# Performance work log

Measured on AMD Instinct MI355X. Metric: run time of the kernel, lower is better.

Reference implementation:

```python
import jax, jax.numpy as jnp
import numpy as np


def setup_inputs() -> dict:
    key = jax.random.key(0)
    ks = jax.random.split(key, 9)
    B, C, H, W = 8, 512, 56, 56
    E = 256  # embed_dim = in_channels / r
    s = 0.02
    return {
        "x": jax.random.normal(ks[0], (B, C, H, W), dtype=jnp.float32),
        "wq": jax.random.normal(ks[1], (E, C), dtype=jnp.float32) * s,
        "bq": jax.random.normal(ks[2], (E,), dtype=jnp.float32) * s,
        "wk": jax.random.normal(ks[3], (E, C), dtype=jnp.float32) * s,
        "bk": jax.random.normal(ks[4], (E,), dtype=jnp.float32) * s,
        "wv": jax.random.normal(ks[5], (E, C), dtype=jnp.float32) * s,
        "bv": jax.random.normal(ks[6], (E,), dtype=jnp.float32) * s,
        "wo": jax.random.normal(ks[7], (C, E), dtype=jnp.float32) * s,
        "bo": jax.random.normal(ks[8], (C,), dtype=jnp.float32) * s,
    }


def reference(x, wq, bq, wk, bk, wv, bv, wo, bo):
    B, C, H, W = x.shape
    N = H * W
    # 1x1 convs == per-pixel linear projections; flatten spatial dims
    xf = x.reshape(B, C, N)                                   # b c n
    q = jnp.einsum("ec,bcn->bne", wq, xf) + bq                # b n e
    k = jnp.einsum("ec,bcn->ben", wk, xf) + bk[None, :, None] # b e n
    v = jnp.einsum("ec,bcn->bne", wv, xf) + bv                # b n e
    attn = jnp.einsum("bne,bem->bnm", q, k) / N               # b n n (unnormalized, /N scale)
    embed = jnp.einsum("bnm,bme->bne", attn, v)               # b n e
    out = jnp.einsum("ce,bne->bcn", wo, embed) + bo[None, :, None]
    return out.reshape(B, C, H, W) + x
```

## Files before the change

kernel.cpp:

```cpp
#include <hip/hip_runtime.h>
#include <hip/hip_bf16.h>


typedef __attribute__((ext_vector_type(8))) __bf16 bf16x8;
typedef __attribute__((ext_vector_type(4))) float floatx4;

struct __align__(8) bh4 { __hip_bfloat16 x, y, z, w; };
struct __align__(16) bh8 { __hip_bfloat16 h[8]; };

__device__ __forceinline__ void load_lds16(const void* g, void* l) {
    __builtin_amdgcn_global_load_lds((const __attribute__((address_space(1))) void*)g,
                                     (__attribute__((address_space(3))) void*)l, 16, 0, 0);
}

__global__ __launch_bounds__(256)
void prep_all(const float* __restrict__ wo, const float* __restrict__ wv,
              const float* __restrict__ wq, const float* __restrict__ wk,
              const float* __restrict__ bq, const float* __restrict__ bk,
              const float* __restrict__ bv,
              __hip_bfloat16* __restrict__ Pdb, __hip_bfloat16* __restrict__ Qtb,
              float* __restrict__ u, float* __restrict__ r, float* __restrict__ w,
              float* __restrict__ kap, float* __restrict__ sv)
{
    const int tid = threadIdx.x;
    if (blockIdx.z == 2) {
        int blk = blockIdx.y * 8 + blockIdx.x;
        if (blk < 2) {
            int c = blk * 256 + tid;
            float su = 0.f, sr = 0.f, sw = 0.f;
            for (int e = 0; e < 256; ++e) {
                su = fmaf(wo[(long long)c * 256 + e], bv[e], su);
                sr = fmaf(bk[e], wq[(long long)e * 512 + c], sr);
                sw = fmaf(wk[(long long)e * 512 + c], bq[e], sw);
            }
            u[c] = su; r[c] = sr; w[c] = sw;
            if (c == 0) {
                float k2 = 0.f;
                for (int e = 0; e < 256; ++e) k2 = fmaf(bk[e], bq[e], k2);
                *kap = k2;
            }
        } else if (blk == 2) {
            float4* p = (float4*)sv;
            for (int i = tid; i < 1024; i += 256) p[i] = make_float4(0.f, 0.f, 0.f, 0.f);
        }
        return;
    }
    __shared__ __align__(16) float As[16][68];
    __shared__ __align__(16) float Bs[16][68];
    const int tx = tid & 15, ty = tid >> 4;
    const int m0 = blockIdx.y * 64, n0 = blockIdx.x * 64;
    const bool doQ = (blockIdx.z == 1);
    const int lk = tid >> 4, lc = (tid & 15) * 4;
    const int lr = tid >> 2, lk4 = (tid & 3) * 4;
    float acc[4][4] = {};
    for (int k0 = 0; k0 < 256; k0 += 16) {
        float4 av, bv4;
        if (doQ) {
            av = *(const float4*)&wq[(long long)(k0 + lk) * 512 + m0 + lc];
            bv4 = *(const float4*)&wk[(long long)(k0 + lk) * 512 + n0 + lc];
        } else {
            av = *(const float4*)&wo[(long long)(m0 + lr) * 256 + k0 + lk4];
            bv4 = *(const float4*)&wv[(long long)(k0 + lk) * 512 + n0 + lc];
        }
        __syncthreads();
        if (doQ) {
            *(float4*)&As[lk][lc] = av;
        } else {
            As[lk4 + 0][lr] = av.x; As[lk4 + 1][lr] = av.y;
            As[lk4 + 2][lr] = av.z; As[lk4 + 3][lr] = av.w;
        }
        *(float4*)&Bs[lk][lc] = bv4;
        __syncthreads();
#pragma unroll
        for (int kk = 0; kk < 16; ++kk) {
            float a[4], b[4];
#pragma unroll
            for (int i = 0; i < 4; ++i) { a[i] = As[kk][ty * 4 + i]; b[i] = Bs[kk][tx * 4 + i]; }
#pragma unroll
            for (int i = 0; i < 4; ++i)
#pragma unroll
                for (int j = 0; j < 4; ++j) acc[i][j] = fmaf(a[i], b[j], acc[i][j]);
        }
    }
    const int mo = m0 + ty * 4, no = n0 + tx * 4;
    if (doQ) {
#pragma unroll
        for (int i = 0; i < 4; ++i)
#pragma unroll
            for (int j = 0; j < 4; ++j)
                Qtb[(long long)(mo + i) * 512 + no + j] = __float2bfloat16(acc[i][j]);
    } else {
#pragma unroll
        for (int i = 0; i < 4; ++i)
#pragma unroll
            for (int j = 0; j < 4; ++j) {
                __hip_bfloat16 v = __float2bfloat16(acc[i][j]);
                Pdb[(long long)(mo + i) * 1024 + no + j] = v;
                Pdb[(long long)(mo + i) * 1024 + no + j + 512] = v;
            }
    }
}

__global__ __launch_bounds__(256)
void transpose_conv(const float* __restrict__ x, __hip_bfloat16* __restrict__ xT,
                    __hip_bfloat16* __restrict__ xnp, float* __restrict__ s)
{
    __shared__ float t[64][65];
    const int b = blockIdx.z;
    const int n0 = blockIdx.x * 64, c0 = blockIdx.y * 64;
    const int tid = threadIdx.x;
    const int nch = tid & 7;
    const int cr  = tid >> 3;
    __hip_bfloat16* xTo = xT + (long long)b * 3200 * 512;
    __hip_bfloat16* xno = xnp + (long long)b * 512 * 3200;

    if (n0 >= 3136) {
        bh8 z8;
#pragma unroll
        for (int k = 0; k < 8; ++k) z8.h[k] = __float2bfloat16(0.f);
#pragma unroll
        for (int pass = 0; pass < 2; ++pass) {
            int rr = cr + 32 * pass;
            *(bh8*)&xno[(long long)(c0 + rr) * 3200 + n0 + nch * 8] = z8;
            *(bh8*)&xTo[(long long)(n0 + rr) * 512 + c0 + nch * 8] = z8;
        }
        return;
    }
    const float* xb = x + (long long)b * 512 * 3136;
#pragma unroll
    for (int pass = 0; pass < 2; ++pass) {
        const int cl = cr + 32 * pass;
        const int c = c0 + cl;
        const float* xr = xb + (long long)c * 3136 + n0 + nch * 8;
        float4 v0 = *(const float4*)xr;
        float4 v1 = *(const float4*)(xr + 4);
        bh8 o;
        o.h[0] = __float2bfloat16(v0.x); o.h[1] = __float2bfloat16(v0.y);
        o.h[2] = __float2bfloat16(v0.z); o.h[3] = __float2bfloat16(v0.w);
        o.h[4] = __float2bfloat16(v1.x); o.h[5] = __float2bfloat16(v1.y);
        o.h[6] = __float2bfloat16(v1.z); o.h[7] = __float2bfloat16(v1.w);
        *(bh8*)&xno[(long long)c * 3200 + n0 + nch * 8] = o;
        const int nl = nch * 8;
        t[nl + 0][cl] = v0.x; t[nl + 1][cl] = v0.y;
        t[nl + 2][cl] = v0.z; t[nl + 3][cl] = v0.w;
        t[nl + 4][cl] = v1.x; t[nl + 5][cl] = v1.y;
        t[nl + 6][cl] = v1.z; t[nl + 7][cl] = v1.w;
        float rs = v0.x + v0.y + v0.z + v0.w + v1.x + v1.y + v1.z + v1.w;
        rs += __shfl_xor(rs, 1, 8);
        rs += __shfl_xor(rs, 2, 8);
        rs += __shfl_xor(rs, 4, 8);
        if (nch == 0) atomicAdd(&s[b * 512 + c], rs);
    }
    __syncthreads();
#pragma unroll
    for (int pass = 0; pass < 2; ++pass) {
        const int nl = cr + 32 * pass;
        const int cc = nch * 8;
        bh8 o;
#pragma unroll
        for (int k = 0; k < 8; ++k) o.h[k] = __float2bfloat16(t[nl][cc + k]);
        *(bh8*)&xTo[(long long)(n0 + nl) * 512 + c0 + cc] = o;
    }
}

__global__ __launch_bounds__(256)
void vec2_kernel(const __hip_bfloat16* __restrict__ T, const __hip_bfloat16* __restrict__ Pdb,
                 const __hip_bfloat16* __restrict__ Qtb, const float* __restrict__ s,
                 const float* __restrict__ u, const float* __restrict__ w,
                 const float* __restrict__ kap, const float* __restrict__ bo,
                 float* __restrict__ ps, float* __restrict__ sq, float* __restrict__ a2)
{
    const int idx = blockIdx.x * 4 + (threadIdx.x >> 6);
    const int lane = threadIdx.x & 63;
    const int b = idx >> 9, c = idx & 511;
    const int j0 = lane * 8;
    const float* sb = s + b * 512;
    float4 s0 = *(const float4*)&sb[j0], s1 = *(const float4*)&sb[j0 + 4];
    float4 w0 = *(const float4*)&w[j0],  w1 = *(const float4*)&w[j0 + 4];
    bf16x8 pv = *(const bf16x8*)&Pdb[(long long)c * 1024 + j0];
    bf16x8 qv = *(const bf16x8*)&Qtb[(long long)c * 512 + j0];
    bf16x8 tv = *(const bf16x8*)&T[(long long)b * 262144 + (long long)c * 512 + j0];
    float sj[8] = {s0.x, s0.y, s0.z, s0.w, s1.x, s1.y, s1.z, s1.w};
    float wj[8] = {w0.x, w0.y, w0.z, w0.w, w1.x, w1.y, w1.z, w1.w};
    float aps = 0.f, asq = 0.f, atw = 0.f, asw = 0.f;
#pragma unroll
    for (int t = 0; t < 8; ++t) {
        aps = fmaf((float)pv[t], sj[t], aps);
        asq = fmaf((float)qv[t], sj[t], asq);
        atw = fmaf((float)tv[t], wj[t], atw);
        asw = fmaf(sj[t], wj[t], asw);
    }
#pragma unroll
    for (int m = 1; m < 64; m <<= 1) {
        aps += __shfl_xor(aps, m);
        asq += __shfl_xor(asq, m);
        atw += __shfl_xor(atw, m);
        asw += __shfl_xor(asw, m);
    }
    if (lane == 0) {
        ps[idx] = aps; sq[idx] = asq;
        float kp = *kap;
        a2[idx] = (atw + u[c] * asw + aps * kp) * (1.f / 3136.f) + u[c] * kp + bo[c];
    }
}

#define SWZ64(row) ((row) & 7)

__global__ __launch_bounds__(256)
void mfma_g(const __hip_bfloat16* __restrict__ A, long long sA, int lda,
            __hip_bfloat16* __restrict__ C, long long sC, int ldc,
            int kLen)
{
    constexpr int BKT = 64;
    constexpr int CPR = BKT / 8;
    constexpr int NC = 64 * CPR / 256;
    __shared__ __hip_bfloat16 As[64 * BKT];
    __shared__ __hip_bfloat16 Bs[64 * BKT];
    const int tid = threadIdx.x;
    const int lane = tid & 63;
    const int w = tid >> 6;
    const int wm = (w >> 1) << 5;
    const int wn = (w & 1) << 5;
    const int ln = lane & 15;
    const int hi = lane >> 4;
    const int bx = blockIdx.x;
    const int batch = bx & 7, ks = bx >> 3;
    int p = blockIdx.y, mt = 0;
    while (p >= 8 - mt) { p -= 8 - mt; ++mt; }
    const int nt = mt + p;
    const int m0 = mt << 6, n0 = nt << 6;
    const long long k0 = (long long)ks * kLen;

    const __hip_bfloat16* gA[NC];
    const __hip_bfloat16* gB[NC];
#pragma unroll
    for (int q0 = 0; q0 < NC; ++q0) {
        int q = tid + 256 * q0;
        int row = q / CPR;
        int c = (q % CPR) ^ SWZ64(row);
        gA[q0] = A + batch * sA + (long long)(m0 + row) * lda + k0 + c * 8;
        gB[q0] = A + batch * sA + (long long)(n0 + row) * lda + k0 + c * 8;
    }
    floatx4 acc[2][2] = {};
    const int nK = kLen / BKT;
    for (int kt = 0; kt < nK; ++kt) {
#pragma unroll
        for (int q0 = 0; q0 < NC; ++q0) {
            load_lds16(gA[q0], As + (tid + 256 * q0) * 8);
            load_lds16(gB[q0], Bs + (tid + 256 * q0) * 8);
            gA[q0] += BKT; gB[q0] += BKT;
        }
        __syncthreads();
#pragma unroll
        for (int kk = 0; kk < BKT / 32; ++kk) {
            const int cidx = kk * 4 + hi;
            bf16x8 af[2], bfr[2];
#pragma unroll
            for (int i = 0; i < 2; ++i) {
                int row = wm + i * 16 + ln;
                af[i] = *(const bf16x8*)(As + row * BKT + ((cidx ^ SWZ64(row)) << 3));
            }
#pragma unroll
            for (int j = 0; j < 2; ++j) {
                int row = wn + j * 16 + ln;
                bfr[j] = *(const bf16x8*)(Bs + row * BKT + ((cidx ^ SWZ64(row)) << 3));
            }
#pragma unroll
            for (int i = 0; i < 2; ++i)
#pragma unroll
                for (int j = 0; j < 2; ++j)
                    acc[i][j] = __builtin_amdgcn_mfma_f32_16x16x32_bf16(af[i], bfr[j], acc[i][j], 0, 0, 0);
        }
        __syncthreads();
    }

    __hip_bfloat16* Cb = C + batch * sC + ks * 512;
#pragma unroll
    for (int i = 0; i < 2; ++i) {
        int mb = m0 + wm + i * 16 + hi * 4;
#pragma unroll
        for (int j = 0; j < 2; ++j) {
            int nl = n0 + wn + j * 16 + ln;
            bh4 mv;
            mv.x = __float2bfloat16(acc[i][j][0]);
            mv.y = __float2bfloat16(acc[i][j][1]);
            mv.z = __float2bfloat16(acc[i][j][2]);
            mv.w = __float2bfloat16(acc[i][j][3]);
            Cb[(long long)(mb + 0) * ldc + nl] = mv.x;
            Cb[(long long)(mb + 1) * ldc + nl] = mv.y;
            Cb[(long long)(mb + 2) * ldc + nl] = mv.z;
            Cb[(long long)(mb + 3) * ldc + nl] = mv.w;
            if (mt != nt)
                *(bh4*)&Cb[(long long)nl * ldc + mb] = mv;
        }
    }
}

template<int MODE>
__global__ __launch_bounds__(256)
void mfma_sm(const __hip_bfloat16* __restrict__ A, long long sA, int lda,
             const __hip_bfloat16* __restrict__ B, long long sB, int ldb,
             __hip_bfloat16* __restrict__ C, long long sC, int ldc,
             const float* __restrict__ pu, const float* __restrict__ pr,
             const float* __restrict__ pps, const float* __restrict__ psq,
             int kLen)
{
    constexpr int BKT = 64;
    constexpr int CPR = BKT / 8;
    constexpr int NC = 64 * CPR / 256;
    __shared__ __hip_bfloat16 As[64 * BKT];
    __shared__ __hip_bfloat16 Bs[64 * BKT];
    const int tid = threadIdx.x;
    const int lane = tid & 63;
    const int w = tid >> 6;
    const int wm = (w >> 1) << 5;
    const int wn = (w & 1) << 5;
    const int ln = lane & 15;
    const int hi = lane >> 4;
    const int batch = blockIdx.x;
    const int m0 = blockIdx.z << 6;
    const int n0 = blockIdx.y << 6;

    const __hip_bfloat16* gA[NC];
    const __hip_bfloat16* gB[NC];
#pragma unroll
    for (int q0 = 0; q0 < NC; ++q0) {
        int q = tid + 256 * q0;
        int row = q / CPR;
        int c = (q % CPR) ^ SWZ64(row);
        gA[q0] = A + batch * sA + (long long)(m0 + row) * lda + c * 8;
        gB[q0] = B + batch * sB + (long long)(n0 + row) * ldb + c * 8;
    }
    floatx4 acc[2][2] = {};
    const int nK = kLen / BKT;
    for (int kt = 0; kt < nK; ++kt) {
#pragma unroll
        for (int q0 = 0; q0 < NC; ++q0) {
            load_lds16(gA[q0], As + (tid + 256 * q0) * 8);
            load_lds16(gB[q0], Bs + (tid + 256 * q0) * 8);
            gA[q0] += BKT; gB[q0] += BKT;
        }
        __syncthreads();
#pragma unroll
        for (int kk = 0; kk < BKT / 32; ++kk) {
            const int cidx = kk * 4 + hi;
            bf16x8 af[2], bfr[2];
#pragma unroll
            for (int i = 0; i < 2; ++i) {
                int row = wm + i * 16 + ln;
                af[i] = *(const bf16x8*)(As + row * BKT + ((cidx ^ SWZ64(row)) << 3));
            }
#pragma unroll
            for (int j = 0; j < 2; ++j) {
                int row = wn + j * 16 + ln;
                bfr[j] = *(const bf16x8*)(Bs + row * BKT + ((cidx ^ SWZ64(row)) << 3));
            }
#pragma unroll
            for (int i = 0; i < 2; ++i)
#pragma unroll
                for (int j = 0; j < 2; ++j)
                    acc[i][j] = __builtin_amdgcn_mfma_f32_16x16x32_bf16(af[i], bfr[j], acc[i][j], 0, 0, 0);
        }
        __syncthreads();
    }

    __hip_bfloat16* Cb = C + batch * sC;
#pragma unroll
    for (int i = 0; i < 2; ++i) {
        int mb = m0 + wm + i * 16 + hi * 4;
#pragma unroll
        for (int r = 0; r < 4; ++r) {
#pragma unroll
            for (int j = 0; j < 2; ++j) {
                int nl = n0 + wn + j * 16 + ln;
                float v = acc[i][j][r];
                if (MODE == 6) {
                    float uu = pu[mb + r], rr = pr[nl];
                    v = (v + uu * psq[batch * 512 + nl] + pps[batch * 512 + mb + r] * rr)
                        * (1.f / 3136.f) + uu * rr;
                }
                Cb[(long long)(mb + r) * ldc + nl] = __float2bfloat16(v);
            }
        }
    }
}

__global__ __launch_bounds__(256)
void mfma64(const __hip_bfloat16* __restrict__ A, long long sA, int lda,
            const __hip_bfloat16* __restrict__ B, long long sB, int ldb,
            float* __restrict__ C, long long sC, int ldc,
            const float* __restrict__ bias, int sBias,
            const float* __restrict__ xres, long long sX,
            int kLen, int Nreal)
{
    constexpr int BKT = 64;
    constexpr int CPR = BKT / 8;
    constexpr int NA = 64 * CPR / 256;
    constexpr int NB = 128 * CPR / 256;
    __shared__ __hip_bfloat16 As[64 * BKT];
    __shared__ __hip_bfloat16 Bs[128 * BKT];
    const int tid = threadIdx.x;
    const int lane = tid & 63;
    const int w = tid >> 6;
    const int ln = lane & 15;
    const int hi = lane >> 4;
    const int batch = blockIdx.x;
    const int m0 = blockIdx.z << 6;
    const int n0 = blockIdx.y << 7;

    const __hip_bfloat16* gA[NA];
    const __hip_bfloat16* gB[NB];
#pragma unroll
    for (int q0 = 0; q0 < NA; ++q0) {
        int q = tid + 256 * q0;
        int row = q / CPR;
        int c = (q % CPR) ^ SWZ64(row);
        gA[q0] = A + batch * sA + (long long)(m0 + row) * lda + c * 8;
    }
#pragma unroll
    for (int q0 = 0; q0 < NB; ++q0) {
        int q = tid + 256 * q0;
        int row = q / CPR;
        int c = (q % CPR) ^ SWZ64(row);
        gB[q0] = B + batch * sB + (long long)(n0 + row) * ldb + c * 8;
    }

    const float* xb = xres + batch * sX;
    float xr[4][4][2];
#pragma unroll
    for (int i = 0; i < 4; ++i)
#pragma unroll
        for (int r = 0; r < 4; ++r)
#pragma unroll
            for (int j = 0; j < 2; ++j) {
                int mb = m0 + i * 16 + hi * 4 + r;
                int nl = n0 + w * 32 + j * 16 + ln;
                int nlc = nl < Nreal ? nl : Nreal - 1;
                xr[i][r][j] = xb[(long long)mb * ldc + nlc];
            }

    floatx4 acc[4][2] = {};
    const int nK = kLen / BKT;
    for (int kt = 0; kt < nK; ++kt) {
#pragma unroll
        for (int q0 = 0; q0 < NA; ++q0) {
            load_lds16(gA[q0], As + (tid + 256 * q0) * 8);
            gA[q0] += BKT;
        }
#pragma unroll
        for (int q0 = 0; q0 < NB; ++q0) {
            load_lds16(gB[q0], Bs + (tid + 256 * q0) * 8);
            gB[q0] += BKT;
        }
        __syncthreads();
#pragma unroll
        for (int kk = 0; kk < BKT / 32; ++kk) {
            const int cidx = kk * 4 + hi;
            bf16x8 af[4], bfr[2];
#pragma unroll
            for (int i = 0; i < 4; ++i) {
                int row = i * 16 + ln;
                af[i] = *(const bf16x8*)(As + row * BKT + ((cidx ^ SWZ64(row)) << 3));
            }
#pragma unroll
            for (int j = 0; j < 2; ++j) {
                int row = w * 32 + j * 16 + ln;
                bfr[j] = *(const bf16x8*)(Bs + row * BKT + ((cidx ^ SWZ64(row)) << 3));
            }
#pragma unroll
            for (int i = 0; i < 4; ++i)
#pragma unroll
                for (int j = 0; j < 2; ++j)
                    acc[i][j] = __builtin_amdgcn_mfma_f32_16x16x32_bf16(af[i], bfr[j], acc[i][j], 0, 0, 0);
        }
        __syncthreads();
    }

    float* Cb = C + batch * sC;
#pragma unroll
    for (int i = 0; i < 4; ++i) {
        int mb = m0 + i * 16 + hi * 4;
#pragma unroll
        for (int r = 0; r < 4; ++r) {
            float bb = bias[batch * sBias + mb + r];
#pragma unroll
            for (int j = 0; j < 2; ++j) {
                int nl = n0 + w * 32 + j * 16 + ln;
                if (nl < Nreal) {
                    Cb[(long long)(mb + r) * ldc + nl] = acc[i][j][r] + bb + xr[i][r][j];
                }
            }
        }
    }
}

extern "C" void kernel_launch(void* const* d_in, const int* in_sizes, int n_in,
                              void* d_out, int out_size, void* d_ws, size_t ws_size,
                              hipStream_t stream)
{
    const float* x  = (const float*)d_in[0];
    const float* wq = (const float*)d_in[1];
    const float* bq = (const float*)d_in[2];
    const float* wk = (const float*)d_in[3];
    const float* bk = (const float*)d_in[4];
    const float* wv = (const float*)d_in[5];
    const float* bv = (const float*)d_in[6];
    const float* wo = (const float*)d_in[7];
    const float* bo = (const float*)d_in[8];
    float* out = (float*)d_out;

    const int N = 3136;
    const long long xs = 512LL * N;
    const long long xs2 = 512LL * 3200;

    char* ob = (char*)d_out;
    __hip_bfloat16* xnp = (__hip_bfloat16*)ob;
    __hip_bfloat16* Gp2 = (__hip_bfloat16*)(ob + 26214400);
    __hip_bfloat16* Tb  = (__hip_bfloat16*)(ob + 34603008);

    char* wsb = (char*)d_ws;
    __hip_bfloat16* xT  = (__hip_bfloat16*)wsb;
    __hip_bfloat16* A2b = (__hip_bfloat16*)(wsb + 26214400);
    __hip_bfloat16* Pdb = (__hip_bfloat16*)(wsb + 30408704);
    __hip_bfloat16* Qtb = (__hip_bfloat16*)(wsb + 31457280);
    float* sv  = (float*)(wsb + 31981568);
    float* u_  = (float*)(wsb + 31997952);
    float* r_  = (float*)(wsb + 32000000);
    float* w_  = (float*)(wsb + 32002048);
    float* kap = (float*)(wsb + 32004096);
    float* ps  = (float*)(wsb + 32004112);
    float* sq  = (float*)(wsb + 32020496);
    float* a2v = (float*)(wsb + 32036880);

    prep_all<<<dim3(8, 8, 3), 256, 0, stream>>>(wo, wv, wq, wk, bq, bk, bv,
                                                Pdb, Qtb, u_, r_, w_, kap, sv);

    transpose_conv<<<dim3(50, 8, 8), 256, 0, stream>>>(x, xT, xnp, sv);

    mfma_g<<<dim3(16, 36), 256, 0, stream>>>(
        xnp, xs2, 3200, Gp2, 524288, 1024, 1600);

    mfma_sm<5><<<dim3(8, 8, 8), 256, 0, stream>>>(
        Pdb, 0, 1024, Gp2, 524288, 1024, Tb, 262144, 512,
        nullptr, nullptr, nullptr, nullptr, 1024);

    vec2_kernel<<<1024, 256, 0, stream>>>(Tb, Pdb, Qtb, sv, u_, w_, kap, bo, ps, sq, a2v);

    mfma_sm<6><<<dim3(8, 8, 8), 256, 0, stream>>>(
        Tb, 262144, 512, Qtb, 0, 512, A2b, 262144, 512,
        u_, r_, ps, sq, 512);

    mfma64<<<dim3(8, 25, 8), 256, 0, stream>>>(
        A2b, 262144, 512, xT, 3200LL * 512, 512,
        out, xs, N, a2v, 512, x, xs, 512, N);
}
```

Measured before the change: 227.5 us.

## Double-buffer LDS tiles in MFMA GEMMs and defer residual loads to epilogue

```diff
diff --git a/kernel.cpp b/kernel.cpp
--- a/kernel.cpp
+++ b/kernel.cpp
@@ -12,6 +12,9 @@
     __builtin_amdgcn_global_load_lds((const __attribute__((address_space(1))) void*)g,
                                      (__attribute__((address_space(3))) void*)l, 16, 0, 0);
 }
+
+#define WAIT_VM(N) __builtin_amdgcn_s_waitcnt(0x0F70 | (N))
+#define BAR() __builtin_amdgcn_s_barrier()
 
 __global__ __launch_bounds__(256)
 void prep_all(const float* __restrict__ wo, const float* __restrict__ wv,
@@ -214,8 +217,8 @@
     constexpr int BKT = 64;
     constexpr int CPR = BKT / 8;
     constexpr int NC = 64 * CPR / 256;
-    __shared__ __hip_bfloat16 As[64 * BKT];
-    __shared__ __hip_bfloat16 Bs[64 * BKT];
+    __shared__ __hip_bfloat16 As[2][64 * BKT];
+    __shared__ __hip_bfloat16 Bs[2][64 * BKT];
     const int tid = threadIdx.x;
     const int lane = tid & 63;
     const int w = tid >> 6;
@@ -243,14 +246,29 @@
     }
     floatx4 acc[2][2] = {};
     const int nK = kLen / BKT;
+
+#pragma unroll
+    for (int q0 = 0; q0 < NC; ++q0) {
+        load_lds16(gA[q0], &As[0][(tid + 256 * q0) * 8]);
+        load_lds16(gB[q0], &Bs[0][(tid + 256 * q0) * 8]);
+        gA[q0] += BKT; gB[q0] += BKT;
+    }
     for (int kt = 0; kt < nK; ++kt) {
-#pragma unroll
-        for (int q0 = 0; q0 < NC; ++q0) {
-            load_lds16(gA[q0], As + (tid + 256 * q0) * 8);
-            load_lds16(gB[q0], Bs + (tid + 256 * q0) * 8);
-            gA[q0] += BKT; gB[q0] += BKT;
-        }
-        __syncthreads();
+        const int pb = kt & 1;
+        if (kt + 1 < nK) {
+#pragma unroll
+            for (int q0 = 0; q0 < NC; ++q0) {
+                load_lds16(gA[q0], &As[pb ^ 1][(tid + 256 * q0) * 8]);
+                load_lds16(gB[q0], &Bs[pb ^ 1][(tid + 256 * q0) * 8]);
+                gA[q0] += BKT; gB[q0] += BKT;
+            }
+            WAIT_VM(4);
+        } else {
+            WAIT_VM(0);
+        }
+        BAR();
+        const __hip_bfloat16* Ab = &As[pb][0];
+        const __hip_bfloat16* Bb = &Bs[pb][0];
 #pragma unroll
         for (int kk = 0; kk < BKT / 32; ++kk) {
             const int cidx = kk * 4 + hi;
@@ -258,12 +276,12 @@
 #pragma unroll
             for (int i = 0; i < 2; ++i) {
                 int row = wm + i * 16 + ln;
-                af[i] = *(const bf16x8*)(As + row * BKT + ((cidx ^ SWZ64(row)) << 3));
+                af[i] = *(const bf16x8*)(Ab + row * BKT + ((cidx ^ SWZ64(row)) << 3));
             }
 #pragma unroll
             for (int j = 0; j < 2; ++j) {
                 int row = wn + j * 16 + ln;
-                bfr[j] = *(const bf16x8*)(Bs + row * BKT + ((cidx ^ SWZ64(row)) << 3));
+                bfr[j] = *(const bf16x8*)(Bb + row * BKT + ((cidx ^ SWZ64(row)) << 3));
             }
 #pragma unroll
             for (int i = 0; i < 2; ++i)
@@ -271,7 +289,7 @@
                 for (int j = 0; j < 2; ++j)
                     acc[i][j] = __builtin_amdgcn_mfma_f32_16x16x32_bf16(af[i], bfr[j], acc[i][j], 0, 0, 0);
         }
-        __syncthreads();
+        BAR();
     }
 
     __hip_bfloat16* Cb = C + batch * sC + ks * 512;
@@ -308,8 +326,8 @@
     constexpr int BKT = 64;
     constexpr int CPR = BKT / 8;
     constexpr int NC = 64 * CPR / 256;
-    __shared__ __hip_bfloat16 As[64 * BKT];
-    __shared__ __hip_bfloat16 Bs[64 * BKT];
+    __shared__ __hip_bfloat16 As[2][64 * BKT];
+    __shared__ __hip_bfloat16 Bs[2][64 * BKT];
     const int tid = threadIdx.x;
     const int lane = tid & 63;
     const int w = tid >> 6;
@@ -333,14 +351,29 @@
     }
     floatx4 acc[2][2] = {};
     const int nK = kLen / BKT;
+
+#pragma unroll
+    for (int q0 = 0; q0 < NC; ++q0) {
+        load_lds16(gA[q0], &As[0][(tid + 256 * q0) * 8]);
+        load_lds16(gB[q0], &Bs[0][(tid + 256 * q0) * 8]);
+        gA[q0] += BKT; gB[q0] += BKT;
+    }
     for (int kt = 0; kt < nK; ++kt) {
-#pragma unroll
-        for (int q0 = 0; q0 < NC; ++q0) {
-            load_lds16(gA[q0], As + (tid + 256 * q0) * 8);
-            load_lds16(gB[q0], Bs + (tid + 256 * q0) * 8);
-            gA[q0] += BKT; gB[q0] += BKT;
-        }
-        __syncthreads();
+        const int pb = kt & 1;
+        if (kt + 1 < nK) {
+#pragma unroll
+            for (int q0 = 0; q0 < NC; ++q0) {
+                load_lds16(gA[q0], &As[pb ^ 1][(tid + 256 * q0) * 8]);
+                load_lds16(gB[q0], &Bs[pb ^ 1][(tid + 256 * q0) * 8]);
+                gA[q0] += BKT; gB[q0] += BKT;
+            }
+            WAIT_VM(4);
+        } else {
+            WAIT_VM(0);
+        }
+        BAR();
+        const __hip_bfloat16* Ab = &As[pb][0];
+        const __hip_bfloat16* Bb = &Bs[pb][0];
 #pragma unroll
         for (int kk = 0; kk < BKT / 32; ++kk) {
             const int cidx = kk * 4 + hi;
@@ -348,12 +381,12 @@
 #pragma unroll
             for (int i = 0; i < 2; ++i) {
                 int row = wm + i * 16 + ln;
-                af[i] = *(const bf16x8*)(As + row * BKT + ((cidx ^ SWZ64(row)) << 3));
+                af[i] = *(const bf16x8*)(Ab + row * BKT + ((cidx ^ SWZ64(row)) << 3));
             }
 #pragma unroll
             for (int j = 0; j < 2; ++j) {
                 int row = wn + j * 16 + ln;
-                bfr[j] = *(const bf16x8*)(Bs + row * BKT + ((cidx ^ SWZ64(row)) << 3));
+                bfr[j] = *(const bf16x8*)(Bb + row * BKT + ((cidx ^ SWZ64(row)) << 3));
             }
 #pragma unroll
             for (int i = 0; i < 2; ++i)
@@ -361,7 +394,7 @@
                 for (int j = 0; j < 2; ++j)
                     acc[i][j] = __builtin_amdgcn_mfma_f32_16x16x32_bf16(af[i], bfr[j], acc[i][j], 0, 0, 0);
         }
-        __syncthreads();
+        BAR();
     }
 
     __hip_bfloat16* Cb = C + batch * sC;
@@ -397,8 +430,8 @@
     constexpr int CPR = BKT / 8;
     constexpr int NA = 64 * CPR / 256;
     constexpr int NB = 128 * CPR / 256;
-    __shared__ __hip_bfloat16 As[64 * BKT];
-    __shared__ __hip_bfloat16 Bs[128 * BKT];
+    __shared__ __hip_bfloat16 As[2][64 * BKT];
+    __shared__ __hip_bfloat16 Bs[2][128 * BKT];
     const int tid = threadIdx.x;
     const int lane = tid & 63;
     const int w = tid >> 6;
@@ -425,34 +458,39 @@
         gB[q0] = B + batch * sB + (long long)(n0 + row) * ldb + c * 8;
     }
 
-    const float* xb = xres + batch * sX;
-    float xr[4][4][2];
-#pragma unroll
-    for (int i = 0; i < 4; ++i)
-#pragma unroll
-        for (int r = 0; r < 4; ++r)
-#pragma unroll
-            for (int j = 0; j < 2; ++j) {
-                int mb = m0 + i * 16 + hi * 4 + r;
-                int nl = n0 + w * 32 + j * 16 + ln;
-                int nlc = nl < Nreal ? nl : Nreal - 1;
-                xr[i][r][j] = xb[(long long)mb * ldc + nlc];
-            }
-
     floatx4 acc[4][2] = {};
     const int nK = kLen / BKT;
+
+#pragma unroll
+    for (int q0 = 0; q0 < NA; ++q0) {
+        load_lds16(gA[q0], &As[0][(tid + 256 * q0) * 8]);
+        gA[q0] += BKT;
+    }
+#pragma unroll
+    for (int q0 = 0; q0 < NB; ++q0) {
+        load_lds16(gB[q0], &Bs[0][(tid + 256 * q0) * 8]);
+        gB[q0] += BKT;
+    }
     for (int kt = 0; kt < nK; ++kt) {
-#pragma unroll
-        for (int q0 = 0; q0 < NA; ++q0) {
-            load_lds16(gA[q0], As + (tid + 256 * q0) * 8);
-            gA[q0] += BKT;
-        }
-#pragma unroll
-        for (int q0 = 0; q0 < NB; ++q0) {
-            load_lds16(gB[q0], Bs + (tid + 256 * q0) * 8);
-            gB[q0] += BKT;
-        }
-        __syncthreads();
+        const int pb = kt & 1;
+        if (kt + 1 < nK) {
+#pragma unroll
+            for (int q0 = 0; q0 < NA; ++q0) {
+                load_lds16(gA[q0], &As[pb ^ 1][(tid + 256 * q0) * 8]);
+                gA[q0] += BKT;
+            }
+#pragma unroll
+            for (int q0 = 0; q0 < NB; ++q0) {
+                load_lds16(gB[q0], &Bs[pb ^ 1][(tid + 256 * q0) * 8]);
+                gB[q0] += BKT;
+            }
+            WAIT_VM(6);
+        } else {
+            WAIT_VM(0);
+        }
+        BAR();
+        const __hip_bfloat16* Ab = &As[pb][0];
+        const __hip_bfloat16* Bb = &Bs[pb][0];
 #pragma unroll
         for (int kk = 0; kk < BKT / 32; ++kk) {
             const int cidx = kk * 4 + hi;
@@ -460,12 +498,12 @@
 #pragma unroll
             for (int i = 0; i < 4; ++i) {
                 int row = i * 16 + ln;
-                af[i] = *(const bf16x8*)(As + row * BKT + ((cidx ^ SWZ64(row)) << 3));
+                af[i] = *(const bf16x8*)(Ab + row * BKT + ((cidx ^ SWZ64(row)) << 3));
             }
 #pragma unroll
             for (int j = 0; j < 2; ++j) {
                 int row = w * 32 + j * 16 + ln;
-                bfr[j] = *(const bf16x8*)(Bs + row * BKT + ((cidx ^ SWZ64(row)) << 3));
+                bfr[j] = *(const bf16x8*)(Bb + row * BKT + ((cidx ^ SWZ64(row)) << 3));
             }
 #pragma unroll
             for (int i = 0; i < 4; ++i)
@@ -473,10 +511,11 @@
                 for (int j = 0; j < 2; ++j)
                     acc[i][j] = __builtin_amdgcn_mfma_f32_16x16x32_bf16(af[i], bfr[j], acc[i][j], 0, 0, 0);
         }
-        __syncthreads();
+        BAR();
     }
 
     float* Cb = C + batch * sC;
+    const float* xb = xres + batch * sX;
 #pragma unroll
     for (int i = 0; i < 4; ++i) {
         int mb = m0 + i * 16 + hi * 4;
@@ -487,7 +526,8 @@
             for (int j = 0; j < 2; ++j) {
                 int nl = n0 + w * 32 + j * 16 + ln;
                 if (nl < Nreal) {
-                    Cb[(long long)(mb + r) * ldc + nl] = acc[i][j][r] + bb + xr[i][r][j];
+                    long long off = (long long)(mb + r) * ldc + nl;
+                    Cb[off] = acc[i][j][r] + bb + xb[off];
                 }
             }
         }
```

Result: slower. 237.9 us (+4.6%).
